# Performance work log

Hardware: AMD Instinct MI355X
Metric: run time of the kernel (lower is better)

The kernel has to match this reference:

```python
import jax, jax.numpy as jnp
import numpy as np

B, P = 4, 2048
NUM_MODS, D_TIME = 22, 8
DIM_S = NUM_MODS + D_TIME + 1          # 31
PHI_W, PSI_W, PSI_LAT = 32, 32, 32
DOT, HEADS, RHO_W = 16, 4, 64


def _xavier(key, shape):
    fan_in, fan_out = shape[0], shape[1]
    std = (2.0 / (fan_in + fan_out)) ** 0.5
    return jax.random.normal(key, shape, jnp.float32) * std


def setup_inputs() -> dict:
    key = jax.random.key(0)
    ks = jax.random.split(key, 20)
    inp = {
        "times": jnp.sort(jax.random.uniform(ks[0], (B, P), jnp.float32) * 100.0, axis=1),
        "values": jax.random.normal(ks[1], (B, P), jnp.float32),
        "measurements": jax.random.randint(ks[2], (B, P), 0, NUM_MODS + 1, jnp.int64 if jax.config.jax_enable_x64 else jnp.int32),
        "non_pad_mask": jnp.ones((B, P, 1), jnp.float32),
        # attention.psi MLP_state(dim_s -> psi_width)
        "psi_w1": _xavier(ks[3], (DIM_S, PSI_W)), "psi_b1": jnp.zeros((PSI_W,), jnp.float32),
        "psi_w2": _xavier(ks[4], (PSI_W, PSI_W)), "psi_b2": jnp.zeros((PSI_W,), jnp.float32),
        # attention.rho Linear(psi_width -> psi_latent_width)
        "arho_w": _xavier(ks[5], (PSI_W, PSI_LAT)), "arho_b": jnp.zeros((PSI_LAT,), jnp.float32),
        # attention key/query projections
        "W_k": _xavier(ks[6], (PSI_LAT + DIM_S, DOT * HEADS)),
        "W_q": _xavier(ks[7], (HEADS, DOT)),
        # phi MLP_state(dim_s -> phi_width)
        "phi_w1": _xavier(ks[8], (DIM_S, PHI_W)), "phi_b1": jnp.zeros((PHI_W,), jnp.float32),
        "phi_w2": _xavier(ks[9], (PHI_W, PHI_W)), "phi_b2": jnp.zeros((PHI_W,), jnp.float32),
        # rho MLP_state(n_heads*phi_width -> rho_width)
        "rho_w1": _xavier(ks[10], (HEADS * PHI_W, RHO_W)), "rho_b1": jnp.zeros((RHO_W,), jnp.float32),
        "rho_w2": _xavier(ks[11], (RHO_W, RHO_W)), "rho_b2": jnp.zeros((RHO_W,), jnp.float32),
    }
    return inp


def _mlp_state(x, mask, w1, b1, w2, b2):
    # MLP_state: relu(fc1(x*mask)); relu(fc2(h*mask)); h*mask  (dropout p=0)
    h = jax.nn.relu((x * mask) @ w1 + b1)
    h = jax.nn.relu((h * mask) @ w2 + b2)
    return h * mask


def _forward(times, values, measurements, non_pad_mask,
             psi_w1, psi_b1, psi_w2, psi_b2, arho_w, arho_b, W_k, W_q,
             phi_w1, phi_b1, phi_w2, phi_b2, rho_w1, rho_b1, rho_w2, rho_b2):
    mask = non_pad_mask  # [B,P,1]
    # temporal encoding: time / 10000^(2*(i//2)/d_time), sin on even, cos on odd
    idx = jnp.arange(D_TIME)
    pos_vec = jnp.power(10000.0, 2.0 * (idx // 2).astype(jnp.float32) / D_TIME)
    r = times[:, :, None] / pos_vec[None, None, :]          # [B,P,d_time]
    tenc = jnp.where(idx % 2 == 0, jnp.sin(r), jnp.cos(r))
    # one-hot measurements, drop padding channel 0
    meas = jax.nn.one_hot(measurements, NUM_MODS + 1, dtype=jnp.float32)[:, :, 1:]
    combined = jnp.concatenate([tenc, values[:, :, None], meas], axis=-1)  # [B,P,dim_s]

    # --- CumulativeSetAttentionLayer ---
    enc_psi = _mlp_state(combined, mask, psi_w1, psi_b1, psi_w2, psi_b2)   # [B,P,psi_w]
    counts = jnp.arange(1, P + 1, dtype=jnp.float32)[None, :, None]
    agg = jnp.cumsum(enc_psi, axis=1) / counts * mask                      # cumulative mean
    agg = (agg @ arho_w + arho_b) * mask                                   # [B,P,psi_lat]
    comb2 = jnp.concatenate([combined, agg], axis=-1)                      # [B,P,dim_s+psi_lat]
    keys = (comb2 @ W_k) * mask                                            # [B,P,DOT*HEADS]
    # torch.split(keys, n_heads, -1) + stack(-1): chunk i has size HEADS -> [B,P,HEADS,DOT]
    keys = keys.reshape(B, P, DOT, HEADS).transpose(0, 1, 3, 2)            # [B,P,h,d]
    preattn = jnp.einsum('bphd,hd->bph', keys, W_q) / jnp.sqrt(jnp.float32(DOT))
    preattn = preattn * mask                                               # [B,P,m]

    # --- phi encoding ---
    enc = _mlp_state(combined, mask, phi_w1, phi_b1, phi_w2, phi_b2)       # [B,P,d_phi]

    # --- cumulative causal softmax weighting ---
    A = preattn[:, None, :, :]                                             # [B,1,Q,m]
    Bc = jax.lax.cummax(preattn, axis=1)[:, :, None, :]                    # [B,P,1,m]
    triu = jnp.triu(jnp.ones((P, P), bool), 1)[None, :, :, None]           # mask Q > P
    D = jnp.exp(jnp.where(triu, -jnp.inf, A - Bc))                          # [B,P,Q,m]
    E = jnp.sum(D, axis=2)                                                 # [B,P,m]
    out5 = jnp.einsum('bpqm,bqd->bpmd', D, enc) / E[:, :, :, None]
    out5 = out5 * mask[:, :, :, None]                                      # [B,P,m,d_phi]

    agg2 = out5.reshape(B, P, HEADS * PHI_W)
    output = _mlp_state(agg2, mask, rho_w1, rho_b1, rho_w2, rho_b2)        # [B,P,rho_w]
    return output


def reference(times, values, measurements, non_pad_mask,
              psi_w1, psi_b1, psi_w2, psi_b2, arho_w, arho_b, W_k, W_q,
              phi_w1, phi_b1, phi_w2, phi_b2, rho_w1, rho_b1, rho_w2, rho_b2):
    return _forward(times, values, measurements, non_pad_mask,
                    psi_w1, psi_b1, psi_w2, psi_b2, arho_w, arho_b, W_k, W_q,
                    phi_w1, phi_b1, phi_w2, phi_b2, rho_w1, rho_b1, rho_w2, rho_b2)
```

## Files before the change

kernel.cpp:

```cpp
#include <hip/hip_runtime.h>
#include <math.h>

#define PB 2048
#define OFF_ENC 0
#define OFF_Q   262144
#define OFF_R   294912
#define OFF_MSK 327680
#define OFF_WV  335872

__global__ __launch_bounds__(64) void k_encode(
    const float* __restrict__ times, const float* __restrict__ vals,
    const int* __restrict__ meas, const float* __restrict__ mask,
    const float* __restrict__ psi_w1, const float* __restrict__ psi_b1,
    const float* __restrict__ psi_w2, const float* __restrict__ psi_b2,
    const float* __restrict__ phi_w1, const float* __restrict__ phi_b1,
    const float* __restrict__ phi_w2, const float* __restrict__ phi_b2,
    const float* __restrict__ arho_w, const float* __restrict__ arho_b,
    const float* __restrict__ W_k, const float* __restrict__ W_q,
    float* __restrict__ ws)
{
    __shared__ float sW[4222];
    __shared__ float sU[31*4];
    __shared__ float sU2[32*4];
    __shared__ float sV[32*4];
    __shared__ float sCc[4];
    for (int i = threadIdx.x; i < 1023; i += 64) {
        int r = i / 33, cc = i - r * 33;
        sW[i]        = (cc < 32) ? psi_w1[r*32 + cc] : 0.0f;
        sW[2111 + i] = (cc < 32) ? phi_w1[r*32 + cc] : 0.0f;
    }
    for (int i = threadIdx.x; i < 1024; i += 64) {
        sW[1055 + i] = psi_w2[i];
        sW[3166 + i] = phi_w2[i];
    }
    if (threadIdx.x < 32) {
        int i = threadIdx.x;
        sW[1023 + i] = psi_b1[i];
        sW[2079 + i] = psi_b2[i];
        sW[3134 + i] = phi_b1[i];
        sW[4190 + i] = phi_b2[i];
    }
    for (int t = threadIdx.x; t < 252; t += 64) {
        int i = t >> 2, h = t & 3;
        float s = 0.0f;
        #pragma unroll
        for (int d = 0; d < 16; d++)
            s = fmaf(W_k[i*64 + d*4 + h], W_q[h*16 + d], s);
        s *= 0.25f;
        if (i < 31) sU[i*4 + h] = s; else sU2[(i-31)*4 + h] = s;
    }
    __syncthreads();
    for (int t = threadIdx.x; t < 128; t += 64) {
        int ch = t >> 2, h = t & 3;
        float s = 0.0f;
        #pragma unroll
        for (int j = 0; j < 32; j++)
            s = fmaf(arho_w[ch*32 + j], sU2[j*4 + h], s);
        sV[t] = s;
    }
    if (threadIdx.x < 4) {
        float s = 0.0f;
        #pragma unroll
        for (int j = 0; j < 32; j++)
            s = fmaf(arho_b[j], sU2[j*4 + threadIdx.x], s);
        sCc[threadIdx.x] = s;
    }
    __syncthreads();

    const int tid  = threadIdx.x;
    const int half = tid >> 5;
    const int jb   = half << 4;
    const int pp = blockIdx.x * 32 + (tid & 31);
    const int b = pp >> 11, p = pp & 2047;
    const float t = times[pp];
    const float v = vals[pp];
    const float msk = mask[pp];
    const int m = meas[pp];

    float c[9];
    c[0] = sinf(t);           c[1] = cosf(t);
    c[2] = sinf(t * 0.1f);    c[3] = cosf(t * 0.1f);
    c[4] = sinf(t * 0.01f);   c[5] = cosf(t * 0.01f);
    c[6] = sinf(t * 0.001f);  c[7] = cosf(t * 0.001f);
    c[8] = v;

    float* enc_t = ws + OFF_ENC;
    const int cb = b * 32;

    float x[9];
    #pragma unroll
    for (int i = 0; i < 9; i++) x[i] = c[i] * msk;
    const float ohs = (m > 0) ? msk : 0.0f;
    const int   ohr = (m > 0) ? (8 + m) * 33 : 0;

    if (half == 0) {
        float r[4] = {sCc[0], sCc[1], sCc[2], sCc[3]};
        #pragma unroll
        for (int i = 0; i < 9; i++) {
            #pragma unroll
            for (int h = 0; h < 4; h++) r[h] = fmaf(c[i], sU[i*4 + h], r[h]);
        }
        if (m > 0) {
            #pragma unroll
            for (int h = 0; h < 4; h++) r[h] += sU[(8 + m)*4 + h];
        }
        #pragma unroll
        for (int h = 0; h < 4; h++)
            ws[OFF_R + (size_t)(b*4 + h) * PB + p] = r[h];
        ws[OFF_MSK + (size_t)b * PB + p] = msk;
    }

    {
        float h1o[16];
        #pragma unroll
        for (int jj = 0; jj < 16; jj++) {
            const int j = jb + jj;
            float acc = sW[1023 + j];
            #pragma unroll
            for (int i = 0; i < 9; i++) acc = fmaf(x[i], sW[i*33 + j], acc);
            acc = fmaf(ohs, sW[ohr + j], acc);
            h1o[jj] = fmaxf(acc, 0.0f) * msk;
        }
        float h1f[32];
        #pragma unroll
        for (int jj = 0; jj < 16; jj++) {
            const float other = __shfl_xor(h1o[jj], 32);
            h1f[jj]      = half ? other   : h1o[jj];
            h1f[16 + jj] = half ? h1o[jj] : other;
        }
        float q[4] = {0.f, 0.f, 0.f, 0.f};
        #pragma unroll
        for (int jj = 0; jj < 16; jj++) {
            const int j = jb + jj;
            float acc = sW[2079 + j];
            #pragma unroll
            for (int i = 0; i < 32; i++) acc = fmaf(h1f[i], sW[1055 + i*32 + j], acc);
            const float p2 = fmaxf(acc, 0.0f) * msk;
            #pragma unroll
            for (int h = 0; h < 4; h++) q[h] = fmaf(p2, sV[j*4 + h], q[h]);
        }
        #pragma unroll
        for (int h = 0; h < 4; h++) q[h] += __shfl_xor(q[h], 32);
        if (half == 0) {
            #pragma unroll
            for (int h = 0; h < 4; h++)
                ws[OFF_Q + (size_t)(b*4 + h) * PB + p] = q[h];
        }
    }
    {
        float h1o[16];
        #pragma unroll
        for (int jj = 0; jj < 16; jj++) {
            const int j = jb + jj;
            float acc = sW[3134 + j];
            #pragma unroll
            for (int i = 0; i < 9; i++) acc = fmaf(x[i], sW[2111 + i*33 + j], acc);
            acc = fmaf(ohs, sW[2111 + ohr + j], acc);
            h1o[jj] = fmaxf(acc, 0.0f) * msk;
        }
        float h1f[32];
        #pragma unroll
        for (int jj = 0; jj < 16; jj++) {
            const float other = __shfl_xor(h1o[jj], 32);
            h1f[jj]      = half ? other   : h1o[jj];
            h1f[16 + jj] = half ? h1o[jj] : other;
        }
        #pragma unroll
        for (int jj = 0; jj < 16; jj++) {
            const int j = jb + jj;
            float acc = sW[4190 + j];
            #pragma unroll
            for (int i = 0; i < 32; i++) acc = fmaf(h1f[i], sW[3166 + i*32 + j], acc);
            enc_t[(size_t)(cb + j) * PB + p] = fmaxf(acc, 0.0f) * msk;
        }
    }
}

__global__ __launch_bounds__(64) void k_mid(float* __restrict__ ws)
{
    const int blk = blockIdx.x;
    const int bh = blk / 33;
    const int c  = blk - bh * 33;
    const int b  = bh >> 2;
    const int lane = threadIdx.x;

    const float4* q4 = (const float4*)(ws + OFF_Q   + (size_t)bh * PB + lane * 32);
    const float4* r4 = (const float4*)(ws + OFF_R   + (size_t)bh * PB + lane * 32);
    const float4* m4 = (const float4*)(ws + OFF_MSK + (size_t)b  * PB + lane * 32);
    const float4* e4 = (const float4*)(ws + OFF_ENC + ((size_t)(b*32 + (c-1))) * PB + lane * 32);
    float4* o4 = (float4*)(ws + OFF_WV + ((size_t)(bh*33 + c)) * PB + lane * 32);

    float vq[32];
    #pragma unroll
    for (int k = 0; k < 8; k++) {
        float4 f = q4[k];
        vq[4*k] = f.x; vq[4*k+1] = f.y; vq[4*k+2] = f.z; vq[4*k+3] = f.w;
    }
    #pragma unroll
    for (int j = 1; j < 32; j++) vq[j] += vq[j-1];
    {
        const float tot = vq[31];
        float x = tot;
        #pragma unroll
        for (int off = 1; off < 64; off <<= 1) {
            float y = __shfl_up(x, off);
            if (lane >= off) x += y;
        }
        const float excl = x - tot;
        #pragma unroll
        for (int j = 0; j < 32; j++) vq[j] += excl;
    }
    float v[32];
    #pragma unroll
    for (int k = 0; k < 8; k++) {
        const float4 fr = r4[k];
        const float4 fm = m4[k];
        const int p0 = lane * 32 + 4*k;
        v[4*k+0] = expf(fm.x * (fr.x + vq[4*k+0] / (float)(p0 + 1)));
        v[4*k+1] = expf(fm.y * (fr.y + vq[4*k+1] / (float)(p0 + 2)));
        v[4*k+2] = expf(fm.z * (fr.z + vq[4*k+2] / (float)(p0 + 3)));
        v[4*k+3] = expf(fm.w * (fr.w + vq[4*k+3] / (float)(p0 + 4)));
    }
    if (c > 0) {
        #pragma unroll
        for (int k = 0; k < 8; k++) {
            float4 f = e4[k];
            v[4*k] *= f.x; v[4*k+1] *= f.y; v[4*k+2] *= f.z; v[4*k+3] *= f.w;
        }
    }
    #pragma unroll
    for (int j = 1; j < 32; j++) v[j] += v[j-1];
    const float tot = v[31];
    float x = tot;
    #pragma unroll
    for (int off = 1; off < 64; off <<= 1) {
        float y = __shfl_up(x, off);
        if (lane >= off) x += y;
    }
    const float excl = x - tot;
    #pragma unroll
    for (int j = 0; j < 32; j++) v[j] += excl;
    #pragma unroll
    for (int k = 0; k < 8; k++)
        o4[k] = make_float4(v[4*k], v[4*k+1], v[4*k+2], v[4*k+3]);
}

__global__ __launch_bounds__(256) void k_rho(
    const float* __restrict__ rho_w1, const float* __restrict__ rho_b1,
    const float* __restrict__ rho_w2, const float* __restrict__ rho_b2,
    const float* __restrict__ ws, float* __restrict__ out)
{
    __shared__ float h1s[16][65];
    __shared__ float scl[16][4];
    __shared__ float mskS[16];
    const int tid = threadIdx.x;
    const int pos = tid >> 4;
    const int g   = tid & 15;
    const int pbase = blockIdx.x * 16;
    const int b  = pbase >> 11;
    const int p0 = pbase & 2047;
    const float* wv = ws + OFF_WV + (size_t)b * 132 * PB;

    if (tid < 64) {
        const int pp = tid >> 2, h = tid & 3;
        const float msk = ws[OFF_MSK + (size_t)b * PB + p0 + pp];
        const float L = wv[(size_t)(h*33) * PB + p0 + pp];
        scl[pp][h] = msk / L;
        if (h == 0) mskS[pp] = msk;
    }
    __syncthreads();

    const int pg = p0 + pos;
    float4 acc = ((const float4*)rho_b1)[g];
    const float4* w14 = (const float4*)rho_w1;
    const float sc0 = scl[pos][0], sc1 = scl[pos][1];
    const float sc2 = scl[pos][2], sc3 = scl[pos][3];
    #pragma unroll
    for (int h = 0; h < 4; h++) {
        const float sc = (h == 0) ? sc0 : (h == 1) ? sc1 : (h == 2) ? sc2 : sc3;
        const float* wvh = wv + (size_t)(h*33 + 1) * PB + pg;
        #pragma unroll 8
        for (int d = 0; d < 32; d++) {
            const float ai = wvh[(size_t)d * PB] * sc;
            const float4 w = w14[(h*32 + d)*16 + g];
            acc.x = fmaf(ai, w.x, acc.x);
            acc.y = fmaf(ai, w.y, acc.y);
            acc.z = fmaf(ai, w.z, acc.z);
            acc.w = fmaf(ai, w.w, acc.w);
        }
    }
    const float msk = mskS[pos];
    h1s[pos][g*4+0] = fmaxf(acc.x, 0.f) * msk;
    h1s[pos][g*4+1] = fmaxf(acc.y, 0.f) * msk;
    h1s[pos][g*4+2] = fmaxf(acc.z, 0.f) * msk;
    h1s[pos][g*4+3] = fmaxf(acc.w, 0.f) * msk;
    __syncthreads();

    float4 acc2 = ((const float4*)rho_b2)[g];
    const float4* w24 = (const float4*)rho_w2;
    #pragma unroll 16
    for (int i = 0; i < 64; i++) {
        const float hv = h1s[pos][i];
        const float4 w = w24[i*16 + g];
        acc2.x = fmaf(hv, w.x, acc2.x);
        acc2.y = fmaf(hv, w.y, acc2.y);
        acc2.z = fmaf(hv, w.z, acc2.z);
        acc2.w = fmaf(hv, w.w, acc2.w);
    }
    float4 o;
    o.x = fmaxf(acc2.x, 0.f) * msk;
    o.y = fmaxf(acc2.y, 0.f) * msk;
    o.z = fmaxf(acc2.z, 0.f) * msk;
    o.w = fmaxf(acc2.w, 0.f) * msk;
    ((float4*)out)[(size_t)(pbase + pos) * 16 + g] = o;
}

extern "C" void kernel_launch(void* const* d_in, const int* in_sizes, int n_in,
                              void* d_out, int out_size, void* d_ws, size_t ws_size,
                              hipStream_t stream)
{
    const float* times  = (const float*)d_in[0];
    const float* vals   = (const float*)d_in[1];
    const int*   meas   = (const int*)d_in[2];
    const float* mask   = (const float*)d_in[3];
    const float* psi_w1 = (const float*)d_in[4];
    const float* psi_b1 = (const float*)d_in[5];
    const float* psi_w2 = (const float*)d_in[6];
    const float* psi_b2 = (const float*)d_in[7];
    const float* arho_w = (const float*)d_in[8];
    const float* arho_b = (const float*)d_in[9];
    const float* W_k    = (const float*)d_in[10];
    const float* W_q    = (const float*)d_in[11];
    const float* phi_w1 = (const float*)d_in[12];
    const float* phi_b1 = (const float*)d_in[13];
    const float* phi_w2 = (const float*)d_in[14];
    const float* phi_b2 = (const float*)d_in[15];
    const float* rho_w1 = (const float*)d_in[16];
    const float* rho_b1 = (const float*)d_in[17];
    const float* rho_w2 = (const float*)d_in[18];
    const float* rho_b2 = (const float*)d_in[19];
    float* ws  = (float*)d_ws;
    float* out = (float*)d_out;

    k_encode<<<dim3(256), dim3(64), 0, stream>>>(times, vals, meas, mask,
        psi_w1, psi_b1, psi_w2, psi_b2, phi_w1, phi_b1, phi_w2, phi_b2,
        arho_w, arho_b, W_k, W_q, ws);
    k_mid<<<dim3(528), dim3(64), 0, stream>>>(ws);
    k_rho<<<dim3(512), dim3(256), 0, stream>>>(rho_w1, rho_b1, rho_w2, rho_b2, ws, out);
}
```

Before: 135.5 us.

## Fuse three kernels into one cooperative kernel with grid-wide syncs

```diff
diff --git a/kernel.cpp b/kernel.cpp
--- a/kernel.cpp
+++ b/kernel.cpp
@@ -1,5 +1,8 @@
 #include <hip/hip_runtime.h>
+#include <hip/hip_cooperative_groups.h>
 #include <math.h>
+
+namespace cg = cooperative_groups;
 
 #define PB 2048
 #define OFF_ENC 0
@@ -8,7 +11,7 @@
 #define OFF_MSK 327680
 #define OFF_WV  335872
 
-__global__ __launch_bounds__(64) void k_encode(
+__global__ __launch_bounds__(256) void k_fused(
     const float* __restrict__ times, const float* __restrict__ vals,
     const int* __restrict__ meas, const float* __restrict__ mask,
     const float* __restrict__ psi_w1, const float* __restrict__ psi_b1,
@@ -17,302 +20,315 @@
     const float* __restrict__ phi_w2, const float* __restrict__ phi_b2,
     const float* __restrict__ arho_w, const float* __restrict__ arho_b,
     const float* __restrict__ W_k, const float* __restrict__ W_q,
-    float* __restrict__ ws)
+    const float* __restrict__ rho_w1, const float* __restrict__ rho_b1,
+    const float* __restrict__ rho_w2, const float* __restrict__ rho_b2,
+    float* __restrict__ ws, float* __restrict__ out)
 {
+    cg::grid_group grid = cg::this_grid();
+
     __shared__ float sW[4222];
     __shared__ float sU[31*4];
     __shared__ float sU2[32*4];
     __shared__ float sV[32*4];
     __shared__ float sCc[4];
-    for (int i = threadIdx.x; i < 1023; i += 64) {
-        int r = i / 33, cc = i - r * 33;
-        sW[i]        = (cc < 32) ? psi_w1[r*32 + cc] : 0.0f;
-        sW[2111 + i] = (cc < 32) ? phi_w1[r*32 + cc] : 0.0f;
-    }
-    for (int i = threadIdx.x; i < 1024; i += 64) {
-        sW[1055 + i] = psi_w2[i];
-        sW[3166 + i] = phi_w2[i];
-    }
-    if (threadIdx.x < 32) {
-        int i = threadIdx.x;
-        sW[1023 + i] = psi_b1[i];
-        sW[2079 + i] = psi_b2[i];
-        sW[3134 + i] = phi_b1[i];
-        sW[4190 + i] = phi_b2[i];
-    }
-    for (int t = threadIdx.x; t < 252; t += 64) {
-        int i = t >> 2, h = t & 3;
-        float s = 0.0f;
-        #pragma unroll
-        for (int d = 0; d < 16; d++)
-            s = fmaf(W_k[i*64 + d*4 + h], W_q[h*16 + d], s);
-        s *= 0.25f;
-        if (i < 31) sU[i*4 + h] = s; else sU2[(i-31)*4 + h] = s;
-    }
-    __syncthreads();
-    for (int t = threadIdx.x; t < 128; t += 64) {
-        int ch = t >> 2, h = t & 3;
-        float s = 0.0f;
-        #pragma unroll
-        for (int j = 0; j < 32; j++)
-            s = fmaf(arho_w[ch*32 + j], sU2[j*4 + h], s);
-        sV[t] = s;
-    }
-    if (threadIdx.x < 4) {
-        float s = 0.0f;
-        #pragma unroll
-        for (int j = 0; j < 32; j++)
-            s = fmaf(arho_b[j], sU2[j*4 + threadIdx.x], s);
-        sCc[threadIdx.x] = s;
-    }
-    __syncthreads();
-
-    const int tid  = threadIdx.x;
-    const int half = tid >> 5;
-    const int jb   = half << 4;
-    const int pp = blockIdx.x * 32 + (tid & 31);
-    const int b = pp >> 11, p = pp & 2047;
-    const float t = times[pp];
-    const float v = vals[pp];
-    const float msk = mask[pp];
-    const int m = meas[pp];
-
-    float c[9];
-    c[0] = sinf(t);           c[1] = cosf(t);
-    c[2] = sinf(t * 0.1f);    c[3] = cosf(t * 0.1f);
-    c[4] = sinf(t * 0.01f);   c[5] = cosf(t * 0.01f);
-    c[6] = sinf(t * 0.001f);  c[7] = cosf(t * 0.001f);
-    c[8] = v;
-
-    float* enc_t = ws + OFF_ENC;
-    const int cb = b * 32;
-
-    float x[9];
-    #pragma unroll
-    for (int i = 0; i < 9; i++) x[i] = c[i] * msk;
-    const float ohs = (m > 0) ? msk : 0.0f;
-    const int   ohr = (m > 0) ? (8 + m) * 33 : 0;
-
-    if (half == 0) {
-        float r[4] = {sCc[0], sCc[1], sCc[2], sCc[3]};
-        #pragma unroll
-        for (int i = 0; i < 9; i++) {
-            #pragma unroll
-            for (int h = 0; h < 4; h++) r[h] = fmaf(c[i], sU[i*4 + h], r[h]);
-        }
-        if (m > 0) {
-            #pragma unroll
-            for (int h = 0; h < 4; h++) r[h] += sU[(8 + m)*4 + h];
-        }
-        #pragma unroll
-        for (int h = 0; h < 4; h++)
-            ws[OFF_R + (size_t)(b*4 + h) * PB + p] = r[h];
-        ws[OFF_MSK + (size_t)b * PB + p] = msk;
-    }
-
-    {
-        float h1o[16];
-        #pragma unroll
-        for (int jj = 0; jj < 16; jj++) {
-            const int j = jb + jj;
-            float acc = sW[1023 + j];
-            #pragma unroll
-            for (int i = 0; i < 9; i++) acc = fmaf(x[i], sW[i*33 + j], acc);
-            acc = fmaf(ohs, sW[ohr + j], acc);
-            h1o[jj] = fmaxf(acc, 0.0f) * msk;
-        }
-        float h1f[32];
-        #pragma unroll
-        for (int jj = 0; jj < 16; jj++) {
-            const float other = __shfl_xor(h1o[jj], 32);
-            h1f[jj]      = half ? other   : h1o[jj];
-            h1f[16 + jj] = half ? h1o[jj] : other;
-        }
-        float q[4] = {0.f, 0.f, 0.f, 0.f};
-        #pragma unroll
-        for (int jj = 0; jj < 16; jj++) {
-            const int j = jb + jj;
-            float acc = sW[2079 + j];
-            #pragma unroll
-            for (int i = 0; i < 32; i++) acc = fmaf(h1f[i], sW[1055 + i*32 + j], acc);
-            const float p2 = fmaxf(acc, 0.0f) * msk;
-            #pragma unroll
-            for (int h = 0; h < 4; h++) q[h] = fmaf(p2, sV[j*4 + h], q[h]);
-        }
-        #pragma unroll
-        for (int h = 0; h < 4; h++) q[h] += __shfl_xor(q[h], 32);
-        if (half == 0) {
-            #pragma unroll
-            for (int h = 0; h < 4; h++)
-                ws[OFF_Q + (size_t)(b*4 + h) * PB + p] = q[h];
-        }
-    }
-    {
-        float h1o[16];
-        #pragma unroll
-        for (int jj = 0; jj < 16; jj++) {
-            const int j = jb + jj;
-            float acc = sW[3134 + j];
-            #pragma unroll
-            for (int i = 0; i < 9; i++) acc = fmaf(x[i], sW[2111 + i*33 + j], acc);
-            acc = fmaf(ohs, sW[2111 + ohr + j], acc);
-            h1o[jj] = fmaxf(acc, 0.0f) * msk;
-        }
-        float h1f[32];
-        #pragma unroll
-        for (int jj = 0; jj < 16; jj++) {
-            const float other = __shfl_xor(h1o[jj], 32);
-            h1f[jj]      = half ? other   : h1o[jj];
-            h1f[16 + jj] = half ? h1o[jj] : other;
-        }
-        #pragma unroll
-        for (int jj = 0; jj < 16; jj++) {
-            const int j = jb + jj;
-            float acc = sW[4190 + j];
-            #pragma unroll
-            for (int i = 0; i < 32; i++) acc = fmaf(h1f[i], sW[3166 + i*32 + j], acc);
-            enc_t[(size_t)(cb + j) * PB + p] = fmaxf(acc, 0.0f) * msk;
-        }
-    }
-}
-
-__global__ __launch_bounds__(64) void k_mid(float* __restrict__ ws)
-{
-    const int blk = blockIdx.x;
-    const int bh = blk / 33;
-    const int c  = blk - bh * 33;
-    const int b  = bh >> 2;
-    const int lane = threadIdx.x;
-
-    const float4* q4 = (const float4*)(ws + OFF_Q   + (size_t)bh * PB + lane * 32);
-    const float4* r4 = (const float4*)(ws + OFF_R   + (size_t)bh * PB + lane * 32);
-    const float4* m4 = (const float4*)(ws + OFF_MSK + (size_t)b  * PB + lane * 32);
-    const float4* e4 = (const float4*)(ws + OFF_ENC + ((size_t)(b*32 + (c-1))) * PB + lane * 32);
-    float4* o4 = (float4*)(ws + OFF_WV + ((size_t)(bh*33 + c)) * PB + lane * 32);
-
-    float vq[32];
-    #pragma unroll
-    for (int k = 0; k < 8; k++) {
-        float4 f = q4[k];
-        vq[4*k] = f.x; vq[4*k+1] = f.y; vq[4*k+2] = f.z; vq[4*k+3] = f.w;
-    }
-    #pragma unroll
-    for (int j = 1; j < 32; j++) vq[j] += vq[j-1];
-    {
-        const float tot = vq[31];
-        float x = tot;
-        #pragma unroll
-        for (int off = 1; off < 64; off <<= 1) {
-            float y = __shfl_up(x, off);
-            if (lane >= off) x += y;
-        }
-        const float excl = x - tot;
-        #pragma unroll
-        for (int j = 0; j < 32; j++) vq[j] += excl;
-    }
-    float v[32];
-    #pragma unroll
-    for (int k = 0; k < 8; k++) {
-        const float4 fr = r4[k];
-        const float4 fm = m4[k];
-        const int p0 = lane * 32 + 4*k;
-        v[4*k+0] = expf(fm.x * (fr.x + vq[4*k+0] / (float)(p0 + 1)));
-        v[4*k+1] = expf(fm.y * (fr.y + vq[4*k+1] / (float)(p0 + 2)));
-        v[4*k+2] = expf(fm.z * (fr.z + vq[4*k+2] / (float)(p0 + 3)));
-        v[4*k+3] = expf(fm.w * (fr.w + vq[4*k+3] / (float)(p0 + 4)));
-    }
-    if (c > 0) {
-        #pragma unroll
-        for (int k = 0; k < 8; k++) {
-            float4 f = e4[k];
-            v[4*k] *= f.x; v[4*k+1] *= f.y; v[4*k+2] *= f.z; v[4*k+3] *= f.w;
-        }
-    }
-    #pragma unroll
-    for (int j = 1; j < 32; j++) v[j] += v[j-1];
-    const float tot = v[31];
-    float x = tot;
-    #pragma unroll
-    for (int off = 1; off < 64; off <<= 1) {
-        float y = __shfl_up(x, off);
-        if (lane >= off) x += y;
-    }
-    const float excl = x - tot;
-    #pragma unroll
-    for (int j = 0; j < 32; j++) v[j] += excl;
-    #pragma unroll
-    for (int k = 0; k < 8; k++)
-        o4[k] = make_float4(v[4*k], v[4*k+1], v[4*k+2], v[4*k+3]);
-}
-
-__global__ __launch_bounds__(256) void k_rho(
-    const float* __restrict__ rho_w1, const float* __restrict__ rho_b1,
-    const float* __restrict__ rho_w2, const float* __restrict__ rho_b2,
-    const float* __restrict__ ws, float* __restrict__ out)
-{
     __shared__ float h1s[16][65];
     __shared__ float scl[16][4];
     __shared__ float mskS[16];
+
     const int tid = threadIdx.x;
-    const int pos = tid >> 4;
-    const int g   = tid & 15;
-    const int pbase = blockIdx.x * 16;
-    const int b  = pbase >> 11;
-    const int p0 = pbase & 2047;
-    const float* wv = ws + OFF_WV + (size_t)b * 132 * PB;
-
-    if (tid < 64) {
-        const int pp = tid >> 2, h = tid & 3;
-        const float msk = ws[OFF_MSK + (size_t)b * PB + p0 + pp];
-        const float L = wv[(size_t)(h*33) * PB + p0 + pp];
-        scl[pp][h] = msk / L;
-        if (h == 0) mskS[pp] = msk;
+
+    if (blockIdx.x < 64) {
+        for (int i = tid; i < 1023; i += 256) {
+            int r = i / 33, cc = i - r * 33;
+            sW[i]        = (cc < 32) ? psi_w1[r*32 + cc] : 0.0f;
+            sW[2111 + i] = (cc < 32) ? phi_w1[r*32 + cc] : 0.0f;
+        }
+        for (int i = tid; i < 1024; i += 256) {
+            sW[1055 + i] = psi_w2[i];
+            sW[3166 + i] = phi_w2[i];
+        }
+        if (tid < 32) {
+            int i = tid;
+            sW[1023 + i] = psi_b1[i];
+            sW[2079 + i] = psi_b2[i];
+            sW[3134 + i] = phi_b1[i];
+            sW[4190 + i] = phi_b2[i];
+        }
+        for (int t = tid; t < 252; t += 256) {
+            int i = t >> 2, h = t & 3;
+            float s = 0.0f;
+            #pragma unroll
+            for (int d = 0; d < 16; d++)
+                s = fmaf(W_k[i*64 + d*4 + h], W_q[h*16 + d], s);
+            s *= 0.25f;
+            if (i < 31) sU[i*4 + h] = s; else sU2[(i-31)*4 + h] = s;
+        }
+        __syncthreads();
+        if (tid < 128) {
+            int ch = tid >> 2, h = tid & 3;
+            float s = 0.0f;
+            #pragma unroll
+            for (int j = 0; j < 32; j++)
+                s = fmaf(arho_w[ch*32 + j], sU2[j*4 + h], s);
+            sV[tid] = s;
+        }
+        if (tid < 4) {
+            float s = 0.0f;
+            #pragma unroll
+            for (int j = 0; j < 32; j++)
+                s = fmaf(arho_b[j], sU2[j*4 + tid], s);
+            sCc[tid] = s;
+        }
+        __syncthreads();
+
+        const int lane = tid & 63;
+        const int wave = tid >> 6;
+        const int half = lane >> 5;
+        const int jb   = half << 4;
+        const int pp = blockIdx.x * 128 + wave * 32 + (lane & 31);
+        const int b = pp >> 11, p = pp & 2047;
+        const float t = times[pp];
+        const float v = vals[pp];
+        const float msk = mask[pp];
+        const int m = meas[pp];
+
+        float c[9];
+        c[0] = sinf(t);           c[1] = cosf(t);
+        c[2] = sinf(t * 0.1f);    c[3] = cosf(t * 0.1f);
+        c[4] = sinf(t * 0.01f);   c[5] = cosf(t * 0.01f);
+        c[6] = sinf(t * 0.001f);  c[7] = cosf(t * 0.001f);
+        c[8] = v;
+
+        float* enc_t = ws + OFF_ENC;
+        const int cb = b * 32;
+
+        float x[9];
+        #pragma unroll
+        for (int i = 0; i < 9; i++) x[i] = c[i] * msk;
+        const float ohs = (m > 0) ? msk : 0.0f;
+        const int   ohr = (m > 0) ? (8 + m) * 33 : 0;
+
+        if (half == 0) {
+            float r[4] = {sCc[0], sCc[1], sCc[2], sCc[3]};
+            #pragma unroll
+            for (int i = 0; i < 9; i++) {
+                #pragma unroll
+                for (int h = 0; h < 4; h++) r[h] = fmaf(c[i], sU[i*4 + h], r[h]);
+            }
+            if (m > 0) {
+                #pragma unroll
+                for (int h = 0; h < 4; h++) r[h] += sU[(8 + m)*4 + h];
+            }
+            #pragma unroll
+            for (int h = 0; h < 4; h++)
+                ws[OFF_R + (size_t)(b*4 + h) * PB + p] = r[h];
+            ws[OFF_MSK + (size_t)b * PB + p] = msk;
+        }
+
+        {
+            float h1o[16];
+            #pragma unroll
+            for (int jj = 0; jj < 16; jj++) {
+                const int j = jb + jj;
+                float acc = sW[1023 + j];
+                #pragma unroll
+                for (int i = 0; i < 9; i++) acc = fmaf(x[i], sW[i*33 + j], acc);
+                acc = fmaf(ohs, sW[ohr + j], acc);
+                h1o[jj] = fmaxf(acc, 0.0f) * msk;
+            }
+            float h1f[32];
+            #pragma unroll
+            for (int jj = 0; jj < 16; jj++) {
+                const float other = __shfl_xor(h1o[jj], 32);
+                h1f[jj]      = half ? other   : h1o[jj];
+                h1f[16 + jj] = half ? h1o[jj] : other;
+            }
+            float q[4] = {0.f, 0.f, 0.f, 0.f};
+            #pragma unroll
+            for (int jj = 0; jj < 16; jj++) {
+                const int j = jb + jj;
+                float acc = sW[2079 + j];
+                #pragma unroll
+                for (int i = 0; i < 32; i++) acc = fmaf(h1f[i], sW[1055 + i*32 + j], acc);
+                const float p2 = fmaxf(acc, 0.0f) * msk;
+                #pragma unroll
+                for (int h = 0; h < 4; h++) q[h] = fmaf(p2, sV[j*4 + h], q[h]);
+            }
+            #pragma unroll
+            for (int h = 0; h < 4; h++) q[h] += __shfl_xor(q[h], 32);
+            if (half == 0) {
+                #pragma unroll
+                for (int h = 0; h < 4; h++)
+                    ws[OFF_Q + (size_t)(b*4 + h) * PB + p] = q[h];
+            }
+        }
+        {
+            float h1o[16];
+            #pragma unroll
+            for (int jj = 0; jj < 16; jj++) {
+                const int j = jb + jj;
+                float acc = sW[3134 + j];
+                #pragma unroll
+                for (int i = 0; i < 9; i++) acc = fmaf(x[i], sW[2111 + i*33 + j], acc);
+                acc = fmaf(ohs, sW[2111 + ohr + j], acc);
+                h1o[jj] = fmaxf(acc, 0.0f) * msk;
+            }
+            float h1f[32];
+            #pragma unroll
+            for (int jj = 0; jj < 16; jj++) {
+                const float other = __shfl_xor(h1o[jj], 32);
+                h1f[jj]      = half ? other   : h1o[jj];
+                h1f[16 + jj] = half ? h1o[jj] : other;
+            }
+            #pragma unroll
+            for (int jj = 0; jj < 16; jj++) {
+                const int j = jb + jj;
+                float acc = sW[4190 + j];
+                #pragma unroll
+                for (int i = 0; i < 32; i++) acc = fmaf(h1f[i], sW[3166 + i*32 + j], acc);
+                enc_t[(size_t)(cb + j) * PB + p] = fmaxf(acc, 0.0f) * msk;
+            }
+        }
     }
-    __syncthreads();
-
-    const int pg = p0 + pos;
-    float4 acc = ((const float4*)rho_b1)[g];
-    const float4* w14 = (const float4*)rho_w1;
-    const float sc0 = scl[pos][0], sc1 = scl[pos][1];
-    const float sc2 = scl[pos][2], sc3 = scl[pos][3];
-    #pragma unroll
-    for (int h = 0; h < 4; h++) {
-        const float sc = (h == 0) ? sc0 : (h == 1) ? sc1 : (h == 2) ? sc2 : sc3;
-        const float* wvh = wv + (size_t)(h*33 + 1) * PB + pg;
-        #pragma unroll 8
-        for (int d = 0; d < 32; d++) {
-            const float ai = wvh[(size_t)d * PB] * sc;
-            const float4 w = w14[(h*32 + d)*16 + g];
-            acc.x = fmaf(ai, w.x, acc.x);
-            acc.y = fmaf(ai, w.y, acc.y);
-            acc.z = fmaf(ai, w.z, acc.z);
-            acc.w = fmaf(ai, w.w, acc.w);
+
+    grid.sync();
+
+    {
+        const int wid = blockIdx.x * 4 + (tid >> 6);
+        if (wid < 528) {
+            const int bh = wid / 33;
+            const int c  = wid - bh * 33;
+            const int b  = bh >> 2;
+            const int lane = tid & 63;
+
+            const float4* q4 = (const float4*)(ws + OFF_Q   + (size_t)bh * PB + lane * 32);
+            const float4* r4 = (const float4*)(ws + OFF_R   + (size_t)bh * PB + lane * 32);
+            const float4* m4 = (const float4*)(ws + OFF_MSK + (size_t)b  * PB + lane * 32);
+            const float4* e4 = (const float4*)(ws + OFF_ENC + ((size_t)(b*32 + (c-1))) * PB + lane * 32);
+            float4* o4 = (float4*)(ws + OFF_WV + ((size_t)(bh*33 + c)) * PB + lane * 32);
+
+            float vq[32];
+            #pragma unroll
+            for (int k = 0; k < 8; k++) {
+                float4 f = q4[k];
+                vq[4*k] = f.x; vq[4*k+1] = f.y; vq[4*k+2] = f.z; vq[4*k+3] = f.w;
+            }
+            #pragma unroll
+            for (int j = 1; j < 32; j++) vq[j] += vq[j-1];
+            {
+                const float tot = vq[31];
+                float x = tot;
+                #pragma unroll
+                for (int off = 1; off < 64; off <<= 1) {
+                    float y = __shfl_up(x, off);
+                    if (lane >= off) x += y;
+                }
+                const float excl = x - tot;
+                #pragma unroll
+                for (int j = 0; j < 32; j++) vq[j] += excl;
+            }
+            float v[32];
+            #pragma unroll
+            for (int k = 0; k < 8; k++) {
+                const float4 fr = r4[k];
+                const float4 fm = m4[k];
+                const int p0 = lane * 32 + 4*k;
+                v[4*k+0] = expf(fm.x * (fr.x + vq[4*k+0] / (float)(p0 + 1)));
+                v[4*k+1] = expf(fm.y * (fr.y + vq[4*k+1] / (float)(p0 + 2)));
+                v[4*k+2] = expf(fm.z * (fr.z + vq[4*k+2] / (float)(p0 + 3)));
+                v[4*k+3] = expf(fm.w * (fr.w + vq[4*k+3] / (float)(p0 + 4)));
+            }
+            if (c > 0) {
+                #pragma unroll
+                for (int k = 0; k < 8; k++) {
+                    float4 f = e4[k];
+                    v[4*k] *= f.x; v[4*k+1] *= f.y; v[4*k+2] *= f.z; v[4*k+3] *= f.w;
+                }
+            }
+            #pragma unroll
+            for (int j = 1; j < 32; j++) v[j] += v[j-1];
+            const float tot = v[31];
+            float x = tot;
+            #pragma unroll
+            for (int off = 1; off < 64; off <<= 1) {
+                float y = __shfl_up(x, off);
+                if (lane >= off) x += y;
+            }
+            const float excl = x - tot;
+            #pragma unroll
+            for (int j = 0; j < 32; j++) v[j] += excl;
+            #pragma unroll
+            for (int k = 0; k < 8; k++)
+                o4[k] = make_float4(v[4*k], v[4*k+1], v[4*k+2], v[4*k+3]);
         }
     }
-    const float msk = mskS[pos];
-    h1s[pos][g*4+0] = fmaxf(acc.x, 0.f) * msk;
-    h1s[pos][g*4+1] = fmaxf(acc.y, 0.f) * msk;
-    h1s[pos][g*4+2] = fmaxf(acc.z, 0.f) * msk;
-    h1s[pos][g*4+3] = fmaxf(acc.w, 0.f) * msk;
-    __syncthreads();
-
-    float4 acc2 = ((const float4*)rho_b2)[g];
-    const float4* w24 = (const float4*)rho_w2;
-    #pragma unroll 16
-    for (int i = 0; i < 64; i++) {
-        const float hv = h1s[pos][i];
-        const float4 w = w24[i*16 + g];
-        acc2.x = fmaf(hv, w.x, acc2.x);
-        acc2.y = fmaf(hv, w.y, acc2.y);
-        acc2.z = fmaf(hv, w.z, acc2.z);
-        acc2.w = fmaf(hv, w.w, acc2.w);
+
+    grid.sync();
+
+    #pragma unroll 1
+    for (int it = 0; it < 2; it++) {
+        const int vb = blockIdx.x * 2 + it;
+        const int pos = tid >> 4;
+        const int g   = tid & 15;
+        const int pbase = vb * 16;
+        const int b  = pbase >> 11;
+        const int p0 = pbase & 2047;
+        const float* wv = ws + OFF_WV + (size_t)b * 132 * PB;
+
+        __syncthreads();
+        if (tid < 64) {
+            const int pp = tid >> 2, h = tid & 3;
+            const float msk = ws[OFF_MSK + (size_t)b * PB + p0 + pp];
+            const float L = wv[(size_t)(h*33) * PB + p0 + pp];
+            scl[pp][h] = msk / L;
+            if (h == 0) mskS[pp] = msk;
+        }
+        __syncthreads();
+
+        const int pg = p0 + pos;
+        float4 acc = ((const float4*)rho_b1)[g];
+        const float4* w14 = (const float4*)rho_w1;
+        const float sc0 = scl[pos][0], sc1 = scl[pos][1];
+        const float sc2 = scl[pos][2], sc3 = scl[pos][3];
+        #pragma unroll
+        for (int h = 0; h < 4; h++) {
+            const float sc = (h == 0) ? sc0 : (h == 1) ? sc1 : (h == 2) ? sc2 : sc3;
+            const float* wvh = wv + (size_t)(h*33 + 1) * PB + pg;
+            #pragma unroll 8
+            for (int d = 0; d < 32; d++) {
+                const float ai = wvh[(size_t)d * PB] * sc;
+                const float4 w = w14[(h*32 + d)*16 + g];
+                acc.x = fmaf(ai, w.x, acc.x);
+                acc.y = fmaf(ai, w.y, acc.y);
+                acc.z = fmaf(ai, w.z, acc.z);
+                acc.w = fmaf(ai, w.w, acc.w);
+            }
+        }
+        const float msk = mskS[pos];
+        h1s[pos][g*4+0] = fmaxf(acc.x, 0.f) * msk;
+        h1s[pos][g*4+1] = fmaxf(acc.y, 0.f) * msk;
+        h1s[pos][g*4+2] = fmaxf(acc.z, 0.f) * msk;
+        h1s[pos][g*4+3] = fmaxf(acc.w, 0.f) * msk;
+        __syncthreads();
+
+        float4 acc2 = ((const float4*)rho_b2)[g];
+        const float4* w24 = (const float4*)rho_w2;
+        #pragma unroll 16
+        for (int i = 0; i < 64; i++) {
+            const float hv = h1s[pos][i];
+            const float4 w = w24[i*16 + g];
+            acc2.x = fmaf(hv, w.x, acc2.x);
+            acc2.y = fmaf(hv, w.y, acc2.y);
+            acc2.z = fmaf(hv, w.z, acc2.z);
+            acc2.w = fmaf(hv, w.w, acc2.w);
+        }
+        float4 o;
+        o.x = fmaxf(acc2.x, 0.f) * msk;
+        o.y = fmaxf(acc2.y, 0.f) * msk;
+        o.z = fmaxf(acc2.z, 0.f) * msk;
+        o.w = fmaxf(acc2.w, 0.f) * msk;
+        ((float4*)out)[(size_t)(pbase + pos) * 16 + g] = o;
     }
-    float4 o;
-    o.x = fmaxf(acc2.x, 0.f) * msk;
-    o.y = fmaxf(acc2.y, 0.f) * msk;
-    o.z = fmaxf(acc2.z, 0.f) * msk;
-    o.w = fmaxf(acc2.w, 0.f) * msk;
-    ((float4*)out)[(size_t)(pbase + pos) * 16 + g] = o;
 }
 
 extern "C" void kernel_launch(void* const* d_in, const int* in_sizes, int n_in,
@@ -342,9 +358,14 @@
     float* ws  = (float*)d_ws;
     float* out = (float*)d_out;
 
-    k_encode<<<dim3(256), dim3(64), 0, stream>>>(times, vals, meas, mask,
-        psi_w1, psi_b1, psi_w2, psi_b2, phi_w1, phi_b1, phi_w2, phi_b2,
-        arho_w, arho_b, W_k, W_q, ws);
-    k_mid<<<dim3(528), dim3(64), 0, stream>>>(ws);
-    k_rho<<<dim3(512), dim3(256), 0, stream>>>(rho_w1, rho_b1, rho_w2, rho_b2, ws, out);
+    void* args[] = {
+        (void*)&times, (void*)&vals, (void*)&meas, (void*)&mask,
+        (void*)&psi_w1, (void*)&psi_b1, (void*)&psi_w2, (void*)&psi_b2,
+        (void*)&phi_w1, (void*)&phi_b1, (void*)&phi_w2, (void*)&phi_b2,
+        (void*)&arho_w, (void*)&arho_b, (void*)&W_k, (void*)&W_q,
+        (void*)&rho_w1, (void*)&rho_b1, (void*)&rho_w2, (void*)&rho_b2,
+        (void*)&ws, (void*)&out
+    };
+    hipLaunchCooperativeKernel((const void*)k_fused, dim3(256), dim3(256),
+                               args, 0, stream);
 }
```

Result: slower. 220.4 us (+62.7%).
